# Optimization experiments

Hardware: AMD Instinct MI355X
Metric: run time of the kernel (lower is better)

Reference implementation:

```python
import jax, jax.numpy as jnp
import numpy as np

B, NPTS = 4, 16384          # clouds, points per cloud (equal-size batches)
DX, DP = 3, 3               # feature dim, coordinate dim -> pos6d is 6-D
RATIO, R, MAX_NB = 0.25, 0.25, 64


def setup_inputs() -> dict:
    key = jax.random.key(0)
    k1, k2 = jax.random.split(key)
    x = jax.random.uniform(k1, (B * NPTS, DX), dtype=jnp.float32)
    pos = jax.random.uniform(k2, (B * NPTS, DP), dtype=jnp.float32)
    # contiguous equal-size batch ids (sorted), as torch_geometric expects
    batch = jnp.repeat(jnp.arange(B, dtype=jnp.int32), NPTS)
    return {"x": x, "pos": pos, "batch": batch}


def _fps(p, m):
    """Farthest point sampling on [n, d] points; returns m int32 indices.
    Deterministic start at index 0 (torch_cluster uses a random start)."""
    n = p.shape[0]

    def step(carry, _):
        mind, last = carry
        d = jnp.sum((p - p[last]) ** 2, axis=-1)       # dist^2 to last pick
        mind = jnp.minimum(mind, d)
        nxt = jnp.argmax(mind).astype(jnp.int32)
        return (mind, nxt), last

    init = (jnp.full((n,), jnp.inf, p.dtype), jnp.int32(0))
    _, idx = jax.lax.scan(step, init, None, length=m)
    return idx                                         # [m]


def reference(x, pos, batch):
    dx = x.shape[1]
    m = int(RATIO * NPTS)                              # centers per cloud
    pos6 = jnp.concatenate([x, pos], axis=-1).reshape(B, NPTS, -1)  # [B,n,6]
    xb = x.reshape(B, NPTS, dx)

    # FPS in 6-D, per cloud
    idx_local = jax.vmap(lambda p: _fps(p, m))(pos6)   # [B, m]
    centers = jnp.take_along_axis(pos6, idx_local[:, :, None], axis=1)  # [B,m,6]

    r2 = R * R
    arange_n = jnp.arange(NPTS, dtype=jnp.int32)
    outs = []
    for b in range(B):  # small fixed loop keeps the [m,n] dist matrix per-cloud
        d2 = jnp.sum((centers[b][:, None, :] - pos6[b][None, :, :]) ** 2, axis=-1)  # [m,n]
        # radius neighbors, capped at MAX_NB, first-in-index-order (torch_cluster-like)
        key_idx = jnp.where(d2 <= r2, arange_n, NPTS)
        neg, cols = jax.lax.top_k(-key_idx, MAX_NB)    # smallest valid indices
        w = (-neg < NPTS).astype(x.dtype)              # [m, MAX_NB] validity
        feats = xb[b][cols]                            # [m, MAX_NB, dx]
        # scatter_mean over row ids == masked mean per center (self always valid)
        outs.append(jnp.einsum('mk,mkd->md', w, feats) / jnp.sum(w, axis=1, keepdims=True))

    x_centers = jnp.concatenate(outs, axis=0)          # [B*m, dx]
    idx_g = (idx_local + (jnp.arange(B, dtype=jnp.int32) * NPTS)[:, None]).reshape(-1)
    return x_centers, pos[idx_g], batch[idx_g]
```

## Files before the change

kernel.cpp:

```cpp
#include <hip/hip_runtime.h>
#include <math.h>

#define BATCH 4
#define NPTS 16384
#define M 4096
#define MAX_NB 64
#define R2F 0.0625f

#define KS 4
#define FPS_T 512
#define WPB (FPS_T / 64)
#define PPB (NPTS / KS)
#define PPT (PPB / FPS_T)
#define SLOT_STRIDE 32

__device__ __forceinline__ float dist2_fma(
    float a0, float a1, float a2, float a3, float a4, float a5,
    float b0, float b1, float b2, float b3, float b4, float b5) {
  float d0 = a0 - b0;
  float s = __builtin_fmaf(d0, d0, 0.0f);
  float d1 = a1 - b1; s = __builtin_fmaf(d1, d1, s);
  float d2 = a2 - b2; s = __builtin_fmaf(d2, d2, s);
  float d3 = a3 - b3; s = __builtin_fmaf(d3, d3, s);
  float d4 = a4 - b4; s = __builtin_fmaf(d4, d4, s);
  float d5 = a5 - b5; s = __builtin_fmaf(d5, d5, s);
  return s;
}

__device__ __forceinline__ float dist2_seq(
    float a0, float a1, float a2, float a3, float a4, float a5,
    float b0, float b1, float b2, float b3, float b4, float b5) {
#pragma clang fp contract(off)
  float d0 = a0 - b0; float s = d0 * d0;
  float d1 = a1 - b1; s = s + d1 * d1;
  float d2 = a2 - b2; s = s + d2 * d2;
  float d3 = a3 - b3; s = s + d3 * d3;
  float d4 = a4 - b4; s = s + d4 * d4;
  float d5 = a5 - b5; s = s + d5 * d5;
  return s;
}

__global__
__attribute__((amdgpu_flat_work_group_size(FPS_T, FPS_T)))
__attribute__((amdgpu_waves_per_eu(2, 2)))
void fps_kernel(
    const float* __restrict__ x, const float* __restrict__ pos,
    float* __restrict__ out, unsigned long long* __restrict__ slots) {
  __shared__ unsigned long long s_wk[2][WPB];
  __shared__ unsigned s_res[2];

  const int b = blockIdx.x & (BATCH - 1);
  const int sblk = blockIdx.x >> 2;
  const int t = threadIdx.x;
  const int w = t >> 6;
  const int lane = t & 63;

  const float* xb = x + (size_t)b * NPTS * 3;
  const float* pb = pos + (size_t)b * NPTS * 3;

  float* out_pos = out + (size_t)BATCH * M * 3;
  int* idx_stash = (int*)(out + (size_t)2 * BATCH * M * 3);

  const int pbase = sblk * PPB;

  if (t < 2 * WPB) s_wk[t >> 3][t & 7] = 0ull;
  if (t == 2 * WPB) { s_res[0] = 0u; s_res[1] = 0u; }

  float c0[PPT], c1[PPT], c2[PPT], c3[PPT], c4[PPT], c5[PPT], mind[PPT];
#pragma unroll
  for (int j = 0; j < PPT; ++j) {
    const int p = pbase + j * FPS_T + t;
    c0[j] = xb[3 * p + 0];
    c1[j] = xb[3 * p + 1];
    c2[j] = xb[3 * p + 2];
    c3[j] = pb[3 * p + 0];
    c4[j] = pb[3 * p + 1];
    c5[j] = pb[3 * p + 2];
    mind[j] = INFINITY;
  }
  __syncthreads();

  int g = 0;
  for (int k = 0; k < M; ++k) {
    const float fx0 = xb[3 * g + 0];
    const float fx1 = xb[3 * g + 1];
    const float fx2 = xb[3 * g + 2];
    const float fx3 = pb[3 * g + 0];
    const float fx4 = pb[3 * g + 1];
    const float fx5 = pb[3 * g + 2];

    if (sblk == 0 && t == 0) {
      idx_stash[b * M + k] = g;
      out_pos[(size_t)(b * M + k) * 3 + 0] = fx3;
      out_pos[(size_t)(b * M + k) * 3 + 1] = fx4;
      out_pos[(size_t)(b * M + k) * 3 + 2] = fx5;
    }
    if (k == M - 1) break;

    float bestv = -1.0f;
    int bestj = 0;
#pragma unroll
    for (int j = 0; j < PPT; ++j) {
      const float d2 = dist2_fma(c0[j], c1[j], c2[j], c3[j], c4[j], c5[j],
                                 fx0, fx1, fx2, fx3, fx4, fx5);
      const float nm = fminf(mind[j], d2);
      mind[j] = nm;
      if (nm > bestv) {
        bestv = nm;
        bestj = j;
      }
    }
    const int besti = pbase + bestj * FPS_T + t;

    unsigned long long kk =
        ((unsigned long long)__float_as_uint(bestv) << 14) |
        (unsigned long long)(unsigned)(16383 - besti);
#pragma unroll
    for (int off = 32; off > 0; off >>= 1) {
      const unsigned long long o = __shfl_xor(kk, off, 64);
      if (o > kk) kk = o;
    }

    const int par = k & 1;
    const unsigned long long want = (unsigned long long)(unsigned)(k + 1);
    const unsigned long long tagged = (want << 46) | kk;

    if (lane == 0) {
      __hip_atomic_store(&s_wk[par][w], tagged, __ATOMIC_RELAXED,
                         __HIP_MEMORY_SCOPE_WORKGROUP);
    }

    if (w == 0) {
      unsigned long long got;
      do {
        got = __hip_atomic_load(&s_wk[par][lane & (WPB - 1)],
                                __ATOMIC_RELAXED,
                                __HIP_MEMORY_SCOPE_WORKGROUP);
      } while ((got >> 46) < want);
#pragma unroll
      for (int off = 1; off < WPB; off <<= 1) {
        const unsigned long long o = __shfl_xor(got, off, 64);
        if (o > got) got = o;
      }
      unsigned long long* sector =
          slots + (size_t)(par * BATCH + b) * SLOT_STRIDE;
      if (lane == 0) {
        __hip_atomic_store(&sector[sblk], got, __ATOMIC_RELAXED,
                           __HIP_MEMORY_SCOPE_AGENT);
      }
      unsigned long long cw = got;
      if (lane < KS) {
        unsigned long long o;
        do {
          o = __hip_atomic_load(&sector[lane], __ATOMIC_RELAXED,
                                __HIP_MEMORY_SCOPE_AGENT);
        } while ((o >> 46) < want);
        if (o > cw) cw = o;
      }
#pragma unroll
      for (int off = 1; off < KS; off <<= 1) {
        const unsigned long long o = __shfl_xor(cw, off, 64);
        if (o > cw) cw = o;
      }
      if (lane == 0) {
        const unsigned word = ((unsigned)(k + 1) << 14) |
                              (unsigned)(16383u - (unsigned)(cw & 0x3FFFull));
        __hip_atomic_store(&s_res[par], word, __ATOMIC_RELAXED,
                           __HIP_MEMORY_SCOPE_WORKGROUP);
      }
    }

    {
      const unsigned wantw = (unsigned)(k + 1) << 14;
      unsigned word;
      do {
        word = __hip_atomic_load(&s_res[par], __ATOMIC_RELAXED,
                                 __HIP_MEMORY_SCOPE_WORKGROUP);
      } while (word < wantw);
      g = __builtin_amdgcn_readfirstlane((int)(word & 0x3FFFu));
    }
  }
}

#define K2_T 256
__global__ __launch_bounds__(K2_T, 4) void nbr_kernel(
    const float* __restrict__ x, const float* __restrict__ pos,
    float* __restrict__ out) {
  const int lane = threadIdx.x & 63;
  const int w = threadIdx.x >> 6;
  const int cbase = blockIdx.x * 16 + w * 4;

  const int* idx_stash = (const int*)(out + (size_t)2 * BATCH * M * 3);
  float* out_x = out;
  float* out_batch = out + (size_t)2 * BATCH * M * 3;

  const int b = cbase / M;
  const float* xb = x + (size_t)b * NPTS * 3;
  const float* pb = pos + (size_t)b * NPTS * 3;

  float cc0[4], cc1[4], cc2[4], cc3[4], cc4[4], cc5[4];
#pragma unroll
  for (int i = 0; i < 4; ++i) {
    const int c = idx_stash[cbase + i];
    cc0[i] = xb[3 * c + 0];
    cc1[i] = xb[3 * c + 1];
    cc2[i] = xb[3 * c + 2];
    cc3[i] = pb[3 * c + 0];
    cc4[i] = pb[3 * c + 1];
    cc5[i] = pb[3 * c + 2];
  }

  float s0[4] = {0, 0, 0, 0}, s1[4] = {0, 0, 0, 0}, s2[4] = {0, 0, 0, 0};
  int cnt[4] = {0, 0, 0, 0};

  for (int p = lane; p < NPTS; p += 64) {
    const float x0 = xb[3 * p + 0];
    const float x1 = xb[3 * p + 1];
    const float x2 = xb[3 * p + 2];
    const float q0 = pb[3 * p + 0];
    const float q1 = pb[3 * p + 1];
    const float q2 = pb[3 * p + 2];
#pragma unroll
    for (int i = 0; i < 4; ++i) {
      const float d2 = dist2_seq(cc0[i], cc1[i], cc2[i], cc3[i], cc4[i],
                                 cc5[i], x0, x1, x2, q0, q1, q2);
      if (d2 <= R2F) {
        cnt[i] += 1;
        s0[i] += x0;
        s1[i] += x1;
        s2[i] += x2;
      }
    }
  }

#pragma unroll
  for (int i = 0; i < 4; ++i) {
#pragma unroll
    for (int off = 32; off > 0; off >>= 1) {
      s0[i] += __shfl_xor(s0[i], off, 64);
      s1[i] += __shfl_xor(s1[i], off, 64);
      s2[i] += __shfl_xor(s2[i], off, 64);
      cnt[i] += __shfl_xor(cnt[i], off, 64);
    }
  }

#pragma unroll
  for (int i = 0; i < 4; ++i) {
    const int total = cnt[i];
    float m0, m1, m2;
    if (total <= MAX_NB) {
      const float denom = (float)total;
      m0 = s0[i] / denom;
      m1 = s1[i] / denom;
      m2 = s2[i] / denom;
    } else {
      const int base = lane * (NPTS / 64);
      int lc = 0;
      for (int p = base; p < base + NPTS / 64; ++p) {
        const float d2 =
            dist2_seq(cc0[i], cc1[i], cc2[i], cc3[i], cc4[i], cc5[i],
                      xb[3 * p + 0], xb[3 * p + 1], xb[3 * p + 2],
                      pb[3 * p + 0], pb[3 * p + 1], pb[3 * p + 2]);
        if (d2 <= R2F) lc += 1;
      }
      int pre = 0;
      for (int l = 0; l < 64; ++l) {
        const int c = __shfl(lc, l, 64);
        if (l < lane) pre += c;
      }
      float t0 = 0, t1 = 0, t2 = 0;
      int r = pre;
      for (int p = base; p < base + NPTS / 64; ++p) {
        const float x0 = xb[3 * p + 0], x1 = xb[3 * p + 1],
                    x2 = xb[3 * p + 2];
        const float d2 =
            dist2_seq(cc0[i], cc1[i], cc2[i], cc3[i], cc4[i], cc5[i], x0, x1,
                      x2, pb[3 * p + 0], pb[3 * p + 1], pb[3 * p + 2]);
        if (d2 <= R2F) {
          if (r < MAX_NB) {
            t0 += x0;
            t1 += x1;
            t2 += x2;
          }
          r += 1;
        }
      }
#pragma unroll
      for (int off = 32; off > 0; off >>= 1) {
        t0 += __shfl_xor(t0, off, 64);
        t1 += __shfl_xor(t1, off, 64);
        t2 += __shfl_xor(t2, off, 64);
      }
      m0 = t0 / 64.0f;
      m1 = t1 / 64.0f;
      m2 = t2 / 64.0f;
    }
    if (lane == i) {
      const int gc = cbase + i;
      out_x[(size_t)gc * 3 + 0] = m0;
      out_x[(size_t)gc * 3 + 1] = m1;
      out_x[(size_t)gc * 3 + 2] = m2;
      out_batch[gc] = (float)b;
    }
  }
}

extern "C" void kernel_launch(void* const* d_in, const int* in_sizes, int n_in,
                              void* d_out, int out_size, void* d_ws,
                              size_t ws_size, hipStream_t stream) {
  (void)in_sizes;
  (void)n_in;
  (void)out_size;
  const float* x = (const float*)d_in[0];
  const float* pos = (const float*)d_in[1];
  float* out = (float*)d_out;

  const size_t slot_bytes =
      (size_t)2 * BATCH * SLOT_STRIDE * sizeof(unsigned long long);
  unsigned long long* slots = (ws_size >= slot_bytes)
                                  ? (unsigned long long*)d_ws
                                  : (unsigned long long*)d_out;
  hipMemsetAsync(slots, 0, slot_bytes, stream);

  fps_kernel<<<BATCH * KS, FPS_T, 0, stream>>>(x, pos, out, slots);
  nbr_kernel<<<(BATCH * M) / 16, K2_T, 0, stream>>>(x, pos, out);
}
```

Before: 7.668 ms.

## Halve FPS block size and have every wave poll global slots directly

The FPS kernel now uses 256 threads per block instead of 512, with one wave per EU, so each thread holds more points in registers. The extra intra-block broadcast through a shared result word is removed. Every wave now spins on the cross-block global slots itself and reduces them, which drops one level of workgroup handoff per FPS step. The cost is more global atomic polling traffic from all waves and more serial work per thread.

```diff
diff --git a/kernel.cpp b/kernel.cpp
--- a/kernel.cpp
+++ b/kernel.cpp
@@ -8,7 +8,7 @@
 #define R2F 0.0625f
 
 #define KS 4
-#define FPS_T 512
+#define FPS_T 256
 #define WPB (FPS_T / 64)
 #define PPB (NPTS / KS)
 #define PPT (PPB / FPS_T)
@@ -42,12 +42,11 @@
 
 __global__
 __attribute__((amdgpu_flat_work_group_size(FPS_T, FPS_T)))
-__attribute__((amdgpu_waves_per_eu(2, 2)))
+__attribute__((amdgpu_waves_per_eu(1, 1)))
 void fps_kernel(
     const float* __restrict__ x, const float* __restrict__ pos,
     float* __restrict__ out, unsigned long long* __restrict__ slots) {
   __shared__ unsigned long long s_wk[2][WPB];
-  __shared__ unsigned s_res[2];
 
   const int b = blockIdx.x & (BATCH - 1);
   const int sblk = blockIdx.x >> 2;
@@ -63,8 +62,7 @@
 
   const int pbase = sblk * PPB;
 
-  if (t < 2 * WPB) s_wk[t >> 3][t & 7] = 0ull;
-  if (t == 2 * WPB) { s_res[0] = 0u; s_res[1] = 0u; }
+  if (t < 2 * WPB) s_wk[t >> 2][t & (WPB - 1)] = 0ull;
 
   float c0[PPT], c1[PPT], c2[PPT], c3[PPT], c4[PPT], c5[PPT], mind[PPT];
 #pragma unroll
@@ -124,6 +122,8 @@
     const int par = k & 1;
     const unsigned long long want = (unsigned long long)(unsigned)(k + 1);
     const unsigned long long tagged = (want << 46) | kk;
+    unsigned long long* sector =
+        slots + (size_t)(par * BATCH + b) * SLOT_STRIDE;
 
     if (lane == 0) {
       __hip_atomic_store(&s_wk[par][w], tagged, __ATOMIC_RELAXED,
@@ -142,43 +142,24 @@
         const unsigned long long o = __shfl_xor(got, off, 64);
         if (o > got) got = o;
       }
-      unsigned long long* sector =
-          slots + (size_t)(par * BATCH + b) * SLOT_STRIDE;
       if (lane == 0) {
         __hip_atomic_store(&sector[sblk], got, __ATOMIC_RELAXED,
                            __HIP_MEMORY_SCOPE_AGENT);
       }
-      unsigned long long cw = got;
-      if (lane < KS) {
-        unsigned long long o;
-        do {
-          o = __hip_atomic_load(&sector[lane], __ATOMIC_RELAXED,
-                                __HIP_MEMORY_SCOPE_AGENT);
-        } while ((o >> 46) < want);
-        if (o > cw) cw = o;
-      }
-#pragma unroll
-      for (int off = 1; off < KS; off <<= 1) {
-        const unsigned long long o = __shfl_xor(cw, off, 64);
-        if (o > cw) cw = o;
-      }
-      if (lane == 0) {
-        const unsigned word = ((unsigned)(k + 1) << 14) |
-                              (unsigned)(16383u - (unsigned)(cw & 0x3FFFull));
-        __hip_atomic_store(&s_res[par], word, __ATOMIC_RELAXED,
-                           __HIP_MEMORY_SCOPE_WORKGROUP);
-      }
-    }
-
-    {
-      const unsigned wantw = (unsigned)(k + 1) << 14;
-      unsigned word;
-      do {
-        word = __hip_atomic_load(&s_res[par], __ATOMIC_RELAXED,
-                                 __HIP_MEMORY_SCOPE_WORKGROUP);
-      } while (word < wantw);
-      g = __builtin_amdgcn_readfirstlane((int)(word & 0x3FFFu));
-    }
+    }
+
+    unsigned long long cw;
+    do {
+      cw = __hip_atomic_load(&sector[lane & (KS - 1)], __ATOMIC_RELAXED,
+                             __HIP_MEMORY_SCOPE_AGENT);
+    } while ((cw >> 46) < want);
+#pragma unroll
+    for (int off = 1; off < KS; off <<= 1) {
+      const unsigned long long o = __shfl_xor(cw, off, 64);
+      if (o > cw) cw = o;
+    }
+    g = __builtin_amdgcn_readfirstlane(
+        16383 - (int)(cw & 0x3FFFull));
   }
 }
 
```

Result: slower. 8.527 ms (+11.2%).
